# Kernel tuning notes

Hardware: AMD Instinct MI355X
Metric: run time of the kernel (lower is better)

Reference implementation:

```python
import jax, jax.numpy as jnp
import numpy as np

# binarize = sign() in forward; standard BNN binarize uses a straight-through
# estimator (gradient clipped to |x|<=1) in backward. Forward math: sign.

def binarize(x):
    return jnp.sign(x)


def setup_inputs() -> dict:
    key = jax.random.key(0)
    k1, k2 = jax.random.split(key)
    M, K, N = 8192, 4096, 4096
    x = jax.random.normal(k1, (M, K), dtype=jnp.float32)
    # xavier-scale init for weight; scale is irrelevant after sign() but kept realistic
    w = jax.random.normal(k2, (K, N), dtype=jnp.float32) * np.sqrt(2.0 / (K + N)).astype(np.float32)
    return {"x": x, "weight": w}


def reference(x, weight):
    # sign-binarize activations and weights, then dense matmul
    xb = binarize(x)            # [M, K] in {-1, 0, +1}
    wb = binarize(weight)       # [K, N]
    return jnp.matmul(xb, wb)   # [M, N]
```

## Files before the change

kernel.cpp:

```cpp
#include <hip/hip_runtime.h>
#include <stdint.h>

#define M_DIM 8192
#define K_DIM 4096
#define N_DIM 4096
#define KB2 2048

using i32x4 = __attribute__((ext_vector_type(4))) int;
using i32x8 = __attribute__((ext_vector_type(8))) int;
using f32x16 = __attribute__((ext_vector_type(16))) float;

typedef const __attribute__((address_space(1))) void g_void;
typedef __attribute__((address_space(3))) void lds_void;

__device__ __forceinline__ void gload_lds16(const void* g, void* l) {
  __builtin_amdgcn_global_load_lds((g_void*)g, (lds_void*)l, 16, 0, 0);
}

__device__ __forceinline__ void barrier_raw() {
  asm volatile("" ::: "memory");
  __builtin_amdgcn_s_barrier();
  asm volatile("" ::: "memory");
}

__device__ __forceinline__ unsigned code4(float v) {
  return v > 0.f ? 0x2u : (v < 0.f ? 0xAu : 0x0u);
}

__global__ void pack_x4_kernel(const float* __restrict__ in,
                               unsigned* __restrict__ out, long n8) {
  long i0 = (long)blockIdx.x * blockDim.x + threadIdx.x;
  long stride = (long)gridDim.x * blockDim.x;
  for (long i = i0; i < n8; i += stride) {
    const float4* p = reinterpret_cast<const float4*>(in + i * 8);
    float4 x0 = p[0], x1 = p[1];
    unsigned w = code4(x0.x) | (code4(x0.y) << 4) | (code4(x0.z) << 8) |
                 (code4(x0.w) << 12) | (code4(x1.x) << 16) |
                 (code4(x1.y) << 20) | (code4(x1.z) << 24) |
                 (code4(x1.w) << 28);
    out[i] = w;
  }
}

__global__ void pack_wt4_kernel(const float* __restrict__ w,
                                unsigned* __restrict__ wt4) {
  __shared__ uint8_t tile[64 * 68];
  int n0 = blockIdx.x * 64;
  int k0 = blockIdx.y * 64;
  int t = threadIdx.x;
#pragma unroll
  for (int i = 0; i < 16; ++i) {
    int flat = t + 256 * i;
    int r = flat >> 6;
    int c = flat & 63;
    tile[c * 68 + r] = (uint8_t)code4(w[(long)(k0 + r) * N_DIM + n0 + c]);
  }
  __syncthreads();
#pragma unroll
  for (int i = 0; i < 2; ++i) {
    int flat = t + 256 * i;
    int nn = flat >> 3;
    int dk = flat & 7;
    const uint8_t* src = &tile[nn * 68 + dk * 8];
    unsigned word = 0;
#pragma unroll
    for (int e = 0; e < 8; ++e) word |= ((unsigned)src[e]) << (4 * e);
    wt4[(long)(n0 + nn) * (K_DIM / 8) + (k0 >> 3) + dk] = word;
  }
}

__device__ __forceinline__ i32x8 lo8(i32x4 r) {
  return __builtin_shufflevector(r, r, 0, 1, 2, 3, -1, -1, -1, -1);
}

#define SCALE1 0x7f7f7f7f

template <int VM, bool ISSUE>
__device__ __forceinline__ void tile_step(
    int t, const uint8_t* __restrict__ Asrc, const uint8_t* __restrict__ Bsrc,
    long off0, long off1, int dstOff, uint8_t* lds, int aRd, int bRd,
    f32x16 (&acc)[4][2]) {
  const uint8_t* buf = lds + (t & 3) * 32768;
  if (ISSUE) {
    long kn = (long)(t + 3) * 64;
    uint8_t* nbuf = lds + ((t + 3) & 3) * 32768;
    gload_lds16(Asrc + off0 + kn, nbuf + dstOff);
    gload_lds16(Asrc + off1 + kn, nbuf + 8192 + dstOff);
    gload_lds16(Bsrc + off0 + kn, nbuf + 16384 + dstOff);
    gload_lds16(Bsrc + off1 + kn, nbuf + 24576 + dstOff);
  }
  i32x4 a0[4], b0[2], a1[4], b1[2];
#pragma unroll
  for (int mi = 0; mi < 4; ++mi)
    a0[mi] = *reinterpret_cast<const i32x4*>(buf + aRd + mi * 2048);
#pragma unroll
  for (int ni = 0; ni < 2; ++ni)
    b0[ni] = *reinterpret_cast<const i32x4*>(buf + bRd + ni * 2048);
#pragma unroll
  for (int mi = 0; mi < 4; ++mi)
    a1[mi] = *reinterpret_cast<const i32x4*>(buf + aRd + mi * 2048 + 1024);
#pragma unroll
  for (int ni = 0; ni < 2; ++ni)
    b1[ni] = *reinterpret_cast<const i32x4*>(buf + bRd + ni * 2048 + 1024);
  asm volatile("s_waitcnt lgkmcnt(6)" ::: "memory");
  __builtin_amdgcn_sched_barrier(0);
  __builtin_amdgcn_s_setprio(1);
#pragma unroll
  for (int mi = 0; mi < 4; ++mi)
#pragma unroll
    for (int ni = 0; ni < 2; ++ni)
      acc[mi][ni] = __builtin_amdgcn_mfma_scale_f32_32x32x64_f8f6f4(
          lo8(a0[mi]), lo8(b0[ni]), acc[mi][ni], 4, 4, 0, SCALE1, 0, SCALE1);
  __builtin_amdgcn_s_setprio(0);
  asm volatile("s_waitcnt lgkmcnt(0)" ::: "memory");
  __builtin_amdgcn_sched_barrier(0);
  __builtin_amdgcn_s_setprio(1);
#pragma unroll
  for (int mi = 0; mi < 4; ++mi)
#pragma unroll
    for (int ni = 0; ni < 2; ++ni)
      acc[mi][ni] = __builtin_amdgcn_mfma_scale_f32_32x32x64_f8f6f4(
          lo8(a1[mi]), lo8(b1[ni]), acc[mi][ni], 4, 4, 0, SCALE1, 0, SCALE1);
  __builtin_amdgcn_s_setprio(0);
  if (VM >= 0) {
    if (VM == 8) asm volatile("s_waitcnt vmcnt(8)" ::: "memory");
    else if (VM == 4) asm volatile("s_waitcnt vmcnt(4)" ::: "memory");
    else asm volatile("s_waitcnt vmcnt(0)" ::: "memory");
    barrier_raw();
  }
}

__global__ __launch_bounds__(512, 2) void gemm_fp4_kernel(
    const uint8_t* __restrict__ A, const uint8_t* __restrict__ B,
    float* __restrict__ C) {
  __shared__ __align__(16) uint8_t lds[4 * 32768];

  int bid = blockIdx.x;
  int wg = (bid & 7) * 64 + (bid >> 3);
  int bm = wg >> 4;
  int bn = wg & 15;

  int tid = threadIdx.x;
  int wid = tid >> 6;
  int lane = tid & 63;
  int wr = wid >> 2;
  int wc = wid & 3;

  const uint8_t* Asrc = A + (long)bm * 256 * KB2;
  const uint8_t* Bsrc = B + (long)bn * 256 * KB2;

  long off0 = (long)((tid >> 7) * 32 + (tid & 31)) * KB2 + (((tid >> 5) & 3) << 4);
  long off1 = off0 + 128L * KB2;
  int dstOff = wid * 1024;

  int aRd = (wr * 4) * 2048 + lane * 16;
  int bRd = 16384 + (wc * 2) * 2048 + lane * 16;

  f32x16 acc[4][2] = {};

#pragma unroll
  for (int t = 0; t < 3; ++t) {
    uint8_t* buf = lds + t * 32768;
    long k0 = (long)t * 64;
    gload_lds16(Asrc + off0 + k0, buf + dstOff);
    gload_lds16(Asrc + off1 + k0, buf + 8192 + dstOff);
    gload_lds16(Bsrc + off0 + k0, buf + 16384 + dstOff);
    gload_lds16(Bsrc + off1 + k0, buf + 24576 + dstOff);
  }
  asm volatile("s_waitcnt vmcnt(8)" ::: "memory");
  barrier_raw();

#pragma unroll 1
  for (int t = 0; t < 29; ++t)
    tile_step<8, true>(t, Asrc, Bsrc, off0, off1, dstOff, lds, aRd, bRd, acc);
  tile_step<4, false>(29, Asrc, Bsrc, off0, off1, dstOff, lds, aRd, bRd, acc);
  tile_step<0, false>(30, Asrc, Bsrc, off0, off1, dstOff, lds, aRd, bRd, acc);
  tile_step<-1, false>(31, Asrc, Bsrc, off0, off1, dstOff, lds, aRd, bRd, acc);

  long row0 = (long)bm * 256 + wr * 128 + ((lane >> 5) << 2);
  long col0 = (long)bn * 256 + wc * 64 + (lane & 31);
#pragma unroll
  for (int mi = 0; mi < 4; ++mi)
#pragma unroll
    for (int ni = 0; ni < 2; ++ni)
#pragma unroll
      for (int r = 0; r < 16; ++r) {
        long row = row0 + mi * 32 + (r & 3) + ((r >> 2) << 3);
        C[row * N_DIM + col0 + ni * 32] = acc[mi][ni][r];
      }
}

extern "C" void kernel_launch(void* const* d_in, const int* in_sizes, int n_in,
                              void* d_out, int out_size, void* d_ws, size_t ws_size,
                              hipStream_t stream) {
  const float* x = (const float*)d_in[0];
  const float* w = (const float*)d_in[1];
  float* out = (float*)d_out;

  uint8_t* x4 = (uint8_t*)d_ws;
  uint8_t* w4t = x4 + (size_t)M_DIM * KB2;

  pack_x4_kernel<<<2048, 256, 0, stream>>>(x, (unsigned*)x4,
                                           (long)M_DIM * K_DIM / 8);
  pack_wt4_kernel<<<dim3(N_DIM / 64, K_DIM / 64), 256, 0, stream>>>(
      w, (unsigned*)w4t);
  gemm_fp4_kernel<<<512, 512, 0, stream>>>(x4, w4t, out);
}
```

Baseline: 141.9 us.

## Prefetch next K-tile LDS fragments into registers during current MFMAs

Restructures the main loop into a register double-buffered pipeline. Each step runs the first MFMA half on fragments already in registers, then syncs and issues the global loads. It then reads the next tile's fragments from LDS before running the second MFMA half, so LDS read latency overlaps with matrix math. The cost is doubled fragment registers, a ping-pong unrolled loop, and changed vmcnt/barrier placement, which could hurt occupancy or introduce buffer-reuse races.

```diff
diff --git a/kernel.cpp b/kernel.cpp
--- a/kernel.cpp
+++ b/kernel.cpp
@@ -75,12 +75,28 @@
 
 #define SCALE1 0x7f7f7f7f
 
-template <int VM, bool ISSUE>
+template <int VM, bool ISSUE, bool READ>
 __device__ __forceinline__ void tile_step(
     int t, const uint8_t* __restrict__ Asrc, const uint8_t* __restrict__ Bsrc,
     long off0, long off1, int dstOff, uint8_t* lds, int aRd, int bRd,
+    i32x4 (&aC)[8], i32x4 (&bC)[4], i32x4 (&aN)[8], i32x4 (&bN)[4],
     f32x16 (&acc)[4][2]) {
-  const uint8_t* buf = lds + (t & 3) * 32768;
+  asm volatile("s_waitcnt lgkmcnt(6)" ::: "memory");
+  __builtin_amdgcn_sched_barrier(0);
+  __builtin_amdgcn_s_setprio(1);
+#pragma unroll
+  for (int mi = 0; mi < 4; ++mi)
+#pragma unroll
+    for (int ni = 0; ni < 2; ++ni)
+      acc[mi][ni] = __builtin_amdgcn_mfma_scale_f32_32x32x64_f8f6f4(
+          lo8(aC[mi]), lo8(bC[ni]), acc[mi][ni], 4, 4, 0, SCALE1, 0, SCALE1);
+  __builtin_amdgcn_s_setprio(0);
+  if (VM >= 0) {
+    if (VM == 8) asm volatile("s_waitcnt vmcnt(8)" ::: "memory");
+    else if (VM == 4) asm volatile("s_waitcnt vmcnt(4)" ::: "memory");
+    else asm volatile("s_waitcnt vmcnt(0)" ::: "memory");
+    barrier_raw();
+  }
   if (ISSUE) {
     long kn = (long)(t + 3) * 64;
     uint8_t* nbuf = lds + ((t + 3) & 3) * 32768;
@@ -89,20 +105,25 @@
     gload_lds16(Bsrc + off0 + kn, nbuf + 16384 + dstOff);
     gload_lds16(Bsrc + off1 + kn, nbuf + 24576 + dstOff);
   }
-  i32x4 a0[4], b0[2], a1[4], b1[2];
-#pragma unroll
-  for (int mi = 0; mi < 4; ++mi)
-    a0[mi] = *reinterpret_cast<const i32x4*>(buf + aRd + mi * 2048);
-#pragma unroll
-  for (int ni = 0; ni < 2; ++ni)
-    b0[ni] = *reinterpret_cast<const i32x4*>(buf + bRd + ni * 2048);
-#pragma unroll
-  for (int mi = 0; mi < 4; ++mi)
-    a1[mi] = *reinterpret_cast<const i32x4*>(buf + aRd + mi * 2048 + 1024);
-#pragma unroll
-  for (int ni = 0; ni < 2; ++ni)
-    b1[ni] = *reinterpret_cast<const i32x4*>(buf + bRd + ni * 2048 + 1024);
-  asm volatile("s_waitcnt lgkmcnt(6)" ::: "memory");
+  if (READ) {
+    const uint8_t* nb = lds + ((t + 1) & 3) * 32768;
+#pragma unroll
+    for (int mi = 0; mi < 4; ++mi)
+      aN[mi] = *reinterpret_cast<const i32x4*>(nb + aRd + mi * 2048);
+#pragma unroll
+    for (int ni = 0; ni < 2; ++ni)
+      bN[ni] = *reinterpret_cast<const i32x4*>(nb + bRd + ni * 2048);
+#pragma unroll
+    for (int mi = 0; mi < 4; ++mi)
+      aN[4 + mi] = *reinterpret_cast<const i32x4*>(nb + aRd + mi * 2048 + 1024);
+#pragma unroll
+    for (int ni = 0; ni < 2; ++ni)
+      bN[2 + ni] = *reinterpret_cast<const i32x4*>(nb + bRd + ni * 2048 + 1024);
+  }
+  if (READ)
+    asm volatile("s_waitcnt lgkmcnt(12)" ::: "memory");
+  else
+    asm volatile("s_waitcnt lgkmcnt(0)" ::: "memory");
   __builtin_amdgcn_sched_barrier(0);
   __builtin_amdgcn_s_setprio(1);
 #pragma unroll
@@ -110,24 +131,9 @@
 #pragma unroll
     for (int ni = 0; ni < 2; ++ni)
       acc[mi][ni] = __builtin_amdgcn_mfma_scale_f32_32x32x64_f8f6f4(
-          lo8(a0[mi]), lo8(b0[ni]), acc[mi][ni], 4, 4, 0, SCALE1, 0, SCALE1);
+          lo8(aC[4 + mi]), lo8(bC[2 + ni]), acc[mi][ni], 4, 4, 0, SCALE1, 0,
+          SCALE1);
   __builtin_amdgcn_s_setprio(0);
-  asm volatile("s_waitcnt lgkmcnt(0)" ::: "memory");
-  __builtin_amdgcn_sched_barrier(0);
-  __builtin_amdgcn_s_setprio(1);
-#pragma unroll
-  for (int mi = 0; mi < 4; ++mi)
-#pragma unroll
-    for (int ni = 0; ni < 2; ++ni)
-      acc[mi][ni] = __builtin_amdgcn_mfma_scale_f32_32x32x64_f8f6f4(
-          lo8(a1[mi]), lo8(b1[ni]), acc[mi][ni], 4, 4, 0, SCALE1, 0, SCALE1);
-  __builtin_amdgcn_s_setprio(0);
-  if (VM >= 0) {
-    if (VM == 8) asm volatile("s_waitcnt vmcnt(8)" ::: "memory");
-    else if (VM == 4) asm volatile("s_waitcnt vmcnt(4)" ::: "memory");
-    else asm volatile("s_waitcnt vmcnt(0)" ::: "memory");
-    barrier_raw();
-  }
 }
 
 __global__ __launch_bounds__(512, 2) void gemm_fp4_kernel(
@@ -156,6 +162,7 @@
   int aRd = (wr * 4) * 2048 + lane * 16;
   int bRd = 16384 + (wc * 2) * 2048 + lane * 16;
 
+  i32x4 aA[8], bA[4], aB[8], bB[4];
   f32x16 acc[4][2] = {};
 
 #pragma unroll
@@ -169,13 +176,34 @@
   }
   asm volatile("s_waitcnt vmcnt(8)" ::: "memory");
   barrier_raw();
+#pragma unroll
+  for (int mi = 0; mi < 4; ++mi)
+    aA[mi] = *reinterpret_cast<const i32x4*>(lds + aRd + mi * 2048);
+#pragma unroll
+  for (int ni = 0; ni < 2; ++ni)
+    bA[ni] = *reinterpret_cast<const i32x4*>(lds + bRd + ni * 2048);
+#pragma unroll
+  for (int mi = 0; mi < 4; ++mi)
+    aA[4 + mi] = *reinterpret_cast<const i32x4*>(lds + aRd + mi * 2048 + 1024);
+#pragma unroll
+  for (int ni = 0; ni < 2; ++ni)
+    bA[2 + ni] = *reinterpret_cast<const i32x4*>(lds + bRd + ni * 2048 + 1024);
 
 #pragma unroll 1
-  for (int t = 0; t < 29; ++t)
-    tile_step<8, true>(t, Asrc, Bsrc, off0, off1, dstOff, lds, aRd, bRd, acc);
-  tile_step<4, false>(29, Asrc, Bsrc, off0, off1, dstOff, lds, aRd, bRd, acc);
-  tile_step<0, false>(30, Asrc, Bsrc, off0, off1, dstOff, lds, aRd, bRd, acc);
-  tile_step<-1, false>(31, Asrc, Bsrc, off0, off1, dstOff, lds, aRd, bRd, acc);
+  for (int t = 0; t < 28; t += 2) {
+    tile_step<4, true, true>(t, Asrc, Bsrc, off0, off1, dstOff, lds, aRd, bRd,
+                             aA, bA, aB, bB, acc);
+    tile_step<4, true, true>(t + 1, Asrc, Bsrc, off0, off1, dstOff, lds, aRd,
+                             bRd, aB, bB, aA, bA, acc);
+  }
+  tile_step<4, true, true>(28, Asrc, Bsrc, off0, off1, dstOff, lds, aRd, bRd,
+                           aA, bA, aB, bB, acc);
+  tile_step<4, false, true>(29, Asrc, Bsrc, off0, off1, dstOff, lds, aRd, bRd,
+                            aB, bB, aA, bA, acc);
+  tile_step<0, false, true>(30, Asrc, Bsrc, off0, off1, dstOff, lds, aRd, bRd,
+                            aA, bA, aB, bB, acc);
+  tile_step<-1, false, false>(31, Asrc, Bsrc, off0, off1, dstOff, lds, aRd,
+                              bRd, aB, bB, aA, bA, acc);
 
   long row0 = (long)bm * 256 + wr * 128 + ((lane >> 5) << 2);
   long col0 = (long)bn * 256 + wc * 64 + (lane & 31);
```

New measurement: 140.2 us. Within noise of the previous version (-1.2%).

## Shrink GEMM tile to 128x256 with triple-buffered LDS and higher occupancy

Applied to the files above, without the earlier changes.

The FP4 MFMA GEMM tile shrinks from 256x256 to 128x256, and the launch goes from 512 to 1024 blocks. The LDS ring drops from 4x32KB stages to 3x24KB stages with prefetch depth 2, and the buffer index becomes a compile-time constant through a 3-way unrolled loop. Launch bounds now request 4 blocks per CU so more waves can hide latency. The costs are less data reuse per tile, more global/L2 traffic for B, and a full lgkmcnt(0) wait before each MFMA group.

```diff
diff --git a/kernel.cpp b/kernel.cpp
--- a/kernel.cpp
+++ b/kernel.cpp
@@ -75,68 +75,52 @@
 
 #define SCALE1 0x7f7f7f7f
 
-template <int VM, bool ISSUE>
+template <int VM, bool ISSUE, int CUR>
 __device__ __forceinline__ void tile_step(
     int t, const uint8_t* __restrict__ Asrc, const uint8_t* __restrict__ Bsrc,
-    long off0, long off1, int dstOff, uint8_t* lds, int aRd, int bRd,
-    f32x16 (&acc)[4][2]) {
-  const uint8_t* buf = lds + (t & 3) * 32768;
+    long offA, long offB0, long offB1, int dstA, int dstB0, int dstB1,
+    uint8_t* lds, int aRd, int bRd, f32x16 (&acc)[2][2]) {
+  const uint8_t* buf = lds + CUR * 24576;
+  constexpr int SN = (CUR + 2) % 3;
   if (ISSUE) {
-    long kn = (long)(t + 3) * 64;
-    uint8_t* nbuf = lds + ((t + 3) & 3) * 32768;
-    gload_lds16(Asrc + off0 + kn, nbuf + dstOff);
-    gload_lds16(Asrc + off1 + kn, nbuf + 8192 + dstOff);
-    gload_lds16(Bsrc + off0 + kn, nbuf + 16384 + dstOff);
-    gload_lds16(Bsrc + off1 + kn, nbuf + 24576 + dstOff);
+    long kn = (long)(t + 2) * 64;
+    uint8_t* nbuf = lds + SN * 24576;
+    gload_lds16(Asrc + offA + kn, nbuf + dstA);
+    gload_lds16(Bsrc + offB0 + kn, nbuf + dstB0);
+    gload_lds16(Bsrc + offB1 + kn, nbuf + dstB1);
   }
-  i32x4 a0[4], b0[2], a1[4], b1[2];
+  i32x4 a[2], b[2];
 #pragma unroll
-  for (int mi = 0; mi < 4; ++mi)
-    a0[mi] = *reinterpret_cast<const i32x4*>(buf + aRd + mi * 2048);
+  for (int h = 0; h < 2; ++h) {
+    a[0] = *reinterpret_cast<const i32x4*>(buf + aRd + h * 1024);
+    a[1] = *reinterpret_cast<const i32x4*>(buf + aRd + 2048 + h * 1024);
+    b[0] = *reinterpret_cast<const i32x4*>(buf + bRd + h * 1024);
+    b[1] = *reinterpret_cast<const i32x4*>(buf + bRd + 2048 + h * 1024);
+    asm volatile("s_waitcnt lgkmcnt(0)" ::: "memory");
+    __builtin_amdgcn_sched_barrier(0);
+    __builtin_amdgcn_s_setprio(1);
 #pragma unroll
-  for (int ni = 0; ni < 2; ++ni)
-    b0[ni] = *reinterpret_cast<const i32x4*>(buf + bRd + ni * 2048);
+    for (int mi = 0; mi < 2; ++mi)
 #pragma unroll
-  for (int mi = 0; mi < 4; ++mi)
-    a1[mi] = *reinterpret_cast<const i32x4*>(buf + aRd + mi * 2048 + 1024);
-#pragma unroll
-  for (int ni = 0; ni < 2; ++ni)
-    b1[ni] = *reinterpret_cast<const i32x4*>(buf + bRd + ni * 2048 + 1024);
-  asm volatile("s_waitcnt lgkmcnt(6)" ::: "memory");
-  __builtin_amdgcn_sched_barrier(0);
-  __builtin_amdgcn_s_setprio(1);
-#pragma unroll
-  for (int mi = 0; mi < 4; ++mi)
-#pragma unroll
-    for (int ni = 0; ni < 2; ++ni)
-      acc[mi][ni] = __builtin_amdgcn_mfma_scale_f32_32x32x64_f8f6f4(
-          lo8(a0[mi]), lo8(b0[ni]), acc[mi][ni], 4, 4, 0, SCALE1, 0, SCALE1);
-  __builtin_amdgcn_s_setprio(0);
-  asm volatile("s_waitcnt lgkmcnt(0)" ::: "memory");
-  __builtin_amdgcn_sched_barrier(0);
-  __builtin_amdgcn_s_setprio(1);
-#pragma unroll
-  for (int mi = 0; mi < 4; ++mi)
-#pragma unroll
-    for (int ni = 0; ni < 2; ++ni)
-      acc[mi][ni] = __builtin_amdgcn_mfma_scale_f32_32x32x64_f8f6f4(
-          lo8(a1[mi]), lo8(b1[ni]), acc[mi][ni], 4, 4, 0, SCALE1, 0, SCALE1);
-  __builtin_amdgcn_s_setprio(0);
+      for (int ni = 0; ni < 2; ++ni)
+        acc[mi][ni] = __builtin_amdgcn_mfma_scale_f32_32x32x64_f8f6f4(
+            lo8(a[mi]), lo8(b[ni]), acc[mi][ni], 4, 4, 0, SCALE1, 0, SCALE1);
+    __builtin_amdgcn_s_setprio(0);
+  }
   if (VM >= 0) {
-    if (VM == 8) asm volatile("s_waitcnt vmcnt(8)" ::: "memory");
-    else if (VM == 4) asm volatile("s_waitcnt vmcnt(4)" ::: "memory");
+    if (VM == 3) asm volatile("s_waitcnt vmcnt(3)" ::: "memory");
     else asm volatile("s_waitcnt vmcnt(0)" ::: "memory");
     barrier_raw();
   }
 }
 
-__global__ __launch_bounds__(512, 2) void gemm_fp4_kernel(
+__global__ __launch_bounds__(512, 4) void gemm_fp4_kernel(
     const uint8_t* __restrict__ A, const uint8_t* __restrict__ B,
     float* __restrict__ C) {
-  __shared__ __align__(16) uint8_t lds[4 * 32768];
+  __shared__ __align__(16) uint8_t lds[3 * 24576];
 
   int bid = blockIdx.x;
-  int wg = (bid & 7) * 64 + (bid >> 3);
+  int wg = (bid & 7) * 128 + (bid >> 3);
   int bm = wg >> 4;
   int bn = wg & 15;
 
@@ -146,41 +130,48 @@
   int wr = wid >> 2;
   int wc = wid & 3;
 
-  const uint8_t* Asrc = A + (long)bm * 256 * KB2;
+  const uint8_t* Asrc = A + (long)bm * 128 * KB2;
   const uint8_t* Bsrc = B + (long)bn * 256 * KB2;
 
-  long off0 = (long)((tid >> 7) * 32 + (tid & 31)) * KB2 + (((tid >> 5) & 3) << 4);
-  long off1 = off0 + 128L * KB2;
-  int dstOff = wid * 1024;
+  long offA = (long)((tid >> 7) * 32 + (tid & 31)) * KB2 + (((tid >> 5) & 3) << 4);
+  long offB0 = offA;
+  long offB1 = offA + 128L * KB2;
+  int dstA = wid * 1024;
+  int dstB0 = 8192 + wid * 1024;
+  int dstB1 = 16384 + wid * 1024;
 
-  int aRd = (wr * 4) * 2048 + lane * 16;
-  int bRd = 16384 + (wc * 2) * 2048 + lane * 16;
+  int aRd = (wr * 2) * 2048 + lane * 16;
+  int bRd = 8192 + (wc * 2) * 2048 + lane * 16;
 
-  f32x16 acc[4][2] = {};
+  f32x16 acc[2][2] = {};
 
-#pragma unroll
-  for (int t = 0; t < 3; ++t) {
-    uint8_t* buf = lds + t * 32768;
-    long k0 = (long)t * 64;
-    gload_lds16(Asrc + off0 + k0, buf + dstOff);
-    gload_lds16(Asrc + off1 + k0, buf + 8192 + dstOff);
-    gload_lds16(Bsrc + off0 + k0, buf + 16384 + dstOff);
-    gload_lds16(Bsrc + off1 + k0, buf + 24576 + dstOff);
-  }
-  asm volatile("s_waitcnt vmcnt(8)" ::: "memory");
+  gload_lds16(Asrc + offA, lds + dstA);
+  gload_lds16(Bsrc + offB0, lds + dstB0);
+  gload_lds16(Bsrc + offB1, lds + dstB1);
+  gload_lds16(Asrc + offA + 64, lds + 24576 + dstA);
+  gload_lds16(Bsrc + offB0 + 64, lds + 24576 + dstB0);
+  gload_lds16(Bsrc + offB1 + 64, lds + 24576 + dstB1);
+  asm volatile("s_waitcnt vmcnt(3)" ::: "memory");
   barrier_raw();
 
 #pragma unroll 1
-  for (int t = 0; t < 29; ++t)
-    tile_step<8, true>(t, Asrc, Bsrc, off0, off1, dstOff, lds, aRd, bRd, acc);
-  tile_step<4, false>(29, Asrc, Bsrc, off0, off1, dstOff, lds, aRd, bRd, acc);
-  tile_step<0, false>(30, Asrc, Bsrc, off0, off1, dstOff, lds, aRd, bRd, acc);
-  tile_step<-1, false>(31, Asrc, Bsrc, off0, off1, dstOff, lds, aRd, bRd, acc);
+  for (int tt = 0; tt < 30; tt += 3) {
+    tile_step<3, true, 0>(tt, Asrc, Bsrc, offA, offB0, offB1, dstA, dstB0,
+                          dstB1, lds, aRd, bRd, acc);
+    tile_step<3, true, 1>(tt + 1, Asrc, Bsrc, offA, offB0, offB1, dstA, dstB0,
+                          dstB1, lds, aRd, bRd, acc);
+    tile_step<3, true, 2>(tt + 2, Asrc, Bsrc, offA, offB0, offB1, dstA, dstB0,
+                          dstB1, lds, aRd, bRd, acc);
+  }
+  tile_step<0, false, 0>(30, Asrc, Bsrc, offA, offB0, offB1, dstA, dstB0,
+                         dstB1, lds, aRd, bRd, acc);
+  tile_step<-1, false, 1>(31, Asrc, Bsrc, offA, offB0, offB1, dstA, dstB0,
+                          dstB1, lds, aRd, bRd, acc);
 
-  long row0 = (long)bm * 256 + wr * 128 + ((lane >> 5) << 2);
+  long row0 = (long)bm * 128 + wr * 64 + ((lane >> 5) << 2);
   long col0 = (long)bn * 256 + wc * 64 + (lane & 31);
 #pragma unroll
-  for (int mi = 0; mi < 4; ++mi)
+  for (int mi = 0; mi < 2; ++mi)
 #pragma unroll
     for (int ni = 0; ni < 2; ++ni)
 #pragma unroll
@@ -204,5 +195,5 @@
                                            (long)M_DIM * K_DIM / 8);
   pack_wt4_kernel<<<dim3(N_DIM / 64, K_DIM / 64), 256, 0, stream>>>(
       w, (unsigned*)w4t);
-  gemm_fp4_kernel<<<512, 512, 0, stream>>>(x4, w4t, out);
+  gemm_fp4_kernel<<<1024, 512, 0, stream>>>(x4, w4t, out);
 }
```

Result: slower. 160.5 us (+13.1%).
